# Optimization experiments

Measured on AMD Instinct MI355X. Metric: run time of the kernel, lower is better.

The kernel has to match this reference:

```python
import jax, jax.numpy as jnp
import numpy as np

DIM = 256
NUM_HEADS = 8
HEAD_DIM = DIM // NUM_HEADS
CPB_HIDDEN = 512
B, N = 2, 2304
TABLE = 9025  # (2*48-1)**2


def _l2norm(t, eps=1e-12):
    # matches torch F.normalize(dim=-1): x / max(||x||, eps)
    n = jnp.sqrt(jnp.sum(t * t, axis=-1, keepdims=True))
    return t / jnp.maximum(n, eps)


def setup_inputs() -> dict:
    key = jax.random.key(0)
    ks = jax.random.split(key, 12)
    x = jax.random.normal(ks[0], (B, N, DIM), dtype=jnp.float32)
    relative_pos_index = jax.random.randint(ks[1], (N, N), 0, TABLE, dtype=jnp.int64)
    relative_coords_table = jax.random.uniform(ks[2], (TABLE, 2), dtype=jnp.float32) * 2.0 - 1.0
    seq_length_scale = jnp.ones((1,), dtype=jnp.float32) * jnp.log2(jnp.float32(N))
    padding_mask = jnp.zeros((B, N), dtype=jnp.int32)
    s = 0.02
    W_qkv = jax.random.normal(ks[3], (3 * DIM, DIM), dtype=jnp.float32) * s
    b_qkv = jnp.zeros((3 * DIM,), dtype=jnp.float32)
    # temperature init: log(exp(1/0.24) - 1) so softplus(temperature) = 1/0.24
    temperature = jnp.full((NUM_HEADS, 1, 1), float(np.log(np.expm1(1.0 / 0.24))), dtype=jnp.float32)
    query_embedding = jax.random.normal(ks[4], (NUM_HEADS, 1, HEAD_DIM), dtype=jnp.float32) * s
    W_proj = jax.random.normal(ks[5], (DIM, DIM), dtype=jnp.float32) * s
    b_proj = jnp.zeros((DIM,), dtype=jnp.float32)
    W_cpb1 = jax.random.normal(ks[6], (CPB_HIDDEN, 2), dtype=jnp.float32) * s
    b_cpb1 = jnp.zeros((CPB_HIDDEN,), dtype=jnp.float32)
    W_cpb2 = jax.random.normal(ks[7], (NUM_HEADS, CPB_HIDDEN), dtype=jnp.float32) * s
    b_cpb2 = jnp.zeros((NUM_HEADS,), dtype=jnp.float32)
    return {
        'x': x, 'relative_pos_index': relative_pos_index,
        'relative_coords_table': relative_coords_table,
        'seq_length_scale': seq_length_scale, 'padding_mask': padding_mask,
        'W_qkv': W_qkv, 'b_qkv': b_qkv, 'temperature': temperature,
        'query_embedding': query_embedding, 'W_proj': W_proj, 'b_proj': b_proj,
        'W_cpb1': W_cpb1, 'b_cpb1': b_cpb1, 'W_cpb2': W_cpb2, 'b_cpb2': b_cpb2,
    }


def reference(x, relative_pos_index, relative_coords_table, seq_length_scale,
              padding_mask, W_qkv, b_qkv, temperature, query_embedding,
              W_proj, b_proj, W_cpb1, b_cpb1, W_cpb2, b_cpb2):
    Bx, Nx, C = x.shape
    h, d = NUM_HEADS, HEAD_DIM
    # qkv projection -> (B, 3h, N, d); first h heads = q, then k, then v
    qkv = (jnp.einsum('bnc,oc->bno', x, W_qkv) + b_qkv)
    qkv = qkv.reshape(Bx, Nx, 3 * h, d).transpose(0, 2, 1, 3)
    q, k, v = qkv[:, :h], qkv[:, h:2 * h], qkv[:, 2 * h:]
    # CPB relative bias: (T,2) -> (T,h) -> (h,N,N) via gather
    hid = jax.nn.relu(relative_coords_table @ W_cpb1.T + b_cpb1)
    tab = hid @ W_cpb2.T + b_cpb2                    # (T, h)
    rel_bias = tab.T[:, relative_pos_index.reshape(-1)].reshape(h, Nx, Nx)
    # cosine-sim attention with learned query embedding + softplus temperature
    scale = jax.nn.softplus(temperature) * seq_length_scale[0]   # (h,1,1)
    qn = (_l2norm(q) + query_embedding) * scale                  # (B,h,N,d)
    kn = _l2norm(k)
    attn = jnp.einsum('bhnd,bhmd->bhnm', qn, kn) + rel_bias
    attn = jax.nn.softmax(attn, axis=-1)
    out = jnp.einsum('bhnm,bhmd->bhnd', attn, v)
    out = out.transpose(0, 2, 1, 3).reshape(Bx, Nx, C)
    out = out @ W_proj.T + b_proj
    return out
```

## Files before the change

### kernel.cpp

```cpp
#include <hip/hip_runtime.h>
#include <math.h>

#define DIMC 256
#define NHEADS 8
#define HDIM 32
#define CPBH 512
#define BB 2
#define NSEQ 2304
#define TAB 9025
#define TABP 9040
#define RTOT (BB*NHEADS*NSEQ)
#define SPLITS 8
#define MSP (NSEQ/SPLITS)
#define PBS 36
#define NCHUNK (NSEQ/32)
#define LOG2E 1.44269504088896340736f

#define NX  (BB*NSEQ*DIMC)
#define NWQ (3*DIMC*DIMC)
#define NWP (DIMC*DIMC)

#define WSPLIT_BLOCKS ((NWQ + NWP) / 1024)
#define IDXP_ELEMS    (NSEQ * NCHUNK * 16)
#define IDXP4_BLOCKS  (IDXP_ELEMS / 1024)
#define CPB_BLOCKS    ((TAB + 63) / 64)

typedef unsigned short ushort;
typedef __attribute__((ext_vector_type(8))) short short8;
typedef __attribute__((ext_vector_type(4))) short short4v;
typedef __attribute__((ext_vector_type(4))) float f32x4;

#define MFMA16(a,b,c) __builtin_amdgcn_mfma_f32_16x16x32_bf16((a),(b),(c),0,0,0)

__device__ __forceinline__ ushort f2bf(float x) {
  unsigned u = __float_as_uint(x);
  u += 0x7FFFu + ((u >> 16) & 1u);
  return (ushort)(u >> 16);
}
__device__ __forceinline__ float bf2f(ushort b) {
  return __uint_as_float(((unsigned)b) << 16);
}
__device__ __forceinline__ float fexp2(float x) {
#if defined(__has_builtin)
#if __has_builtin(__builtin_amdgcn_exp2f)
  return __builtin_amdgcn_exp2f(x);
#else
  return exp2f(x);
#endif
#else
  return exp2f(x);
#endif
}
__device__ __forceinline__ unsigned pack_trunc(float p0, float p1) {
  return __builtin_amdgcn_perm(__float_as_uint(p1), __float_as_uint(p0), 0x07060302u);
}
__device__ __forceinline__ void cvt8(const float* __restrict__ p, short8* hi, short8* lo) {
  float4 v0 = *(const float4*)p;
  float4 v1 = *(const float4*)(p + 4);
  float vv[8] = {v0.x, v0.y, v0.z, v0.w, v1.x, v1.y, v1.z, v1.w};
  short8 h, l;
#pragma unroll
  for (int i = 0; i < 8; ++i) {
    ushort hh = f2bf(vv[i]);
    h[i] = (short)hh;
    l[i] = (short)f2bf(vv[i] - bf2f(hh));
  }
  *hi = h; *lo = l;
}

__global__ void setup_kernel(const float* __restrict__ wq, const float* __restrict__ wp,
                             const int* __restrict__ idx,
                             const float* __restrict__ tbl, const float* __restrict__ W1,
                             const float* __restrict__ b1, const float* __restrict__ W2,
                             const float* __restrict__ b2,
                             ushort* __restrict__ wqh, ushort* __restrict__ wql,
                             ushort* __restrict__ wph, ushort* __restrict__ wpl,
                             unsigned* __restrict__ idxP, ushort* __restrict__ tabBf) {
  __shared__ float w1b[CPBH * 4];
  __shared__ float w2t[CPBH * NHEADS];
  __shared__ float part[4][64][NHEADS];
  int blk = blockIdx.x;
  int tid = threadIdx.x;
  if (blk < CPB_BLOCKS) {
    for (int i = tid; i < CPBH; i += 256) {
      w1b[i * 4 + 0] = W1[2 * i];
      w1b[i * 4 + 1] = W1[2 * i + 1];
      w1b[i * 4 + 2] = b1[i];
      w1b[i * 4 + 3] = 0.f;
    }
    for (int i = tid; i < CPBH * NHEADS; i += 256)
      w2t[(i & (CPBH - 1)) * NHEADS + (i >> 9)] = W2[i];
    int tl = tid & 63, jc = tid >> 6;
    int t = blk * 64 + tl;
    bool valid = t < TAB;
    float c0 = 0.f, c1 = 0.f;
    if (valid) { c0 = tbl[2 * t]; c1 = tbl[2 * t + 1]; }
    __syncthreads();
    float acc[NHEADS];
#pragma unroll
    for (int h = 0; h < NHEADS; ++h) acc[h] = 0.f;
    for (int j = jc * 128; j < jc * 128 + 128; ++j) {
      float4 wv = *(const float4*)&w1b[j * 4];
      float hid = fmaxf(fmaf(c0, wv.x, fmaf(c1, wv.y, wv.z)), 0.f);
      float4 wa = *(const float4*)&w2t[j * NHEADS];
      float4 wb = *(const float4*)&w2t[j * NHEADS + 4];
      acc[0] = fmaf(hid, wa.x, acc[0]);
      acc[1] = fmaf(hid, wa.y, acc[1]);
      acc[2] = fmaf(hid, wa.z, acc[2]);
      acc[3] = fmaf(hid, wa.w, acc[3]);
      acc[4] = fmaf(hid, wb.x, acc[4]);
      acc[5] = fmaf(hid, wb.y, acc[5]);
      acc[6] = fmaf(hid, wb.z, acc[6]);
      acc[7] = fmaf(hid, wb.w, acc[7]);
    }
#pragma unroll
    for (int h = 0; h < NHEADS; ++h) part[jc][tl][h] = acc[h];
    __syncthreads();
    if (jc == 0 && valid) {
#pragma unroll
      for (int h = 0; h < NHEADS; ++h) {
        float s = part[0][tl][h] + part[1][tl][h] + part[2][tl][h] + part[3][tl][h] + b2[h];
        tabBf[h * TABP + t] = f2bf(s * LOG2E);
      }
    }
  } else if (blk < CPB_BLOCKS + WSPLIT_BLOCKS) {
    int i = ((blk - CPB_BLOCKS) * 256 + tid) * 4;
    const float* src; ushort *hi, *lo; int j;
    if (i < NWQ) { src = wq; hi = wqh; lo = wql; j = i; }
    else         { src = wp; hi = wph; lo = wpl; j = i - NWQ; }
    float4 v = *(const float4*)&src[j];
    ushort h0 = f2bf(v.x), h1 = f2bf(v.y), h2 = f2bf(v.z), h3 = f2bf(v.w);
    uint2 hp, lp;
    hp.x = (unsigned)h0 | ((unsigned)h1 << 16);
    hp.y = (unsigned)h2 | ((unsigned)h3 << 16);
    lp.x = (unsigned)f2bf(v.x - bf2f(h0)) | ((unsigned)f2bf(v.y - bf2f(h1)) << 16);
    lp.y = (unsigned)f2bf(v.z - bf2f(h2)) | ((unsigned)f2bf(v.w - bf2f(h3)) << 16);
    *(uint2*)&hi[j] = hp;
    *(uint2*)&lo[j] = lp;
  } else {
    int t4 = (blk - CPB_BLOCKS - WSPLIT_BLOCKS) * 256 + tid;
    int cc4 = (t4 & 3) * 4;
    int ch = (t4 >> 2) % NCHUNK;
    int n = t4 / (4 * NCHUNK);
    int mbase = ch * 32 + cc4;
    int4 a = *(const int4*)&idx[(size_t)n * NSEQ + mbase];
    int4 b = *(const int4*)&idx[(size_t)n * NSEQ + mbase + 16];
    uint4 o;
    o.x = (unsigned)a.x | ((unsigned)b.x << 16);
    o.y = (unsigned)a.y | ((unsigned)b.y << 16);
    o.z = (unsigned)a.z | ((unsigned)b.z << 16);
    o.w = (unsigned)a.w | ((unsigned)b.w << 16);
    *(uint4*)&idxP[((size_t)n * NCHUNK + ch) * 16 + cc4] = o;
  }
}

__launch_bounds__(256)
__global__ void gemm_qkv(const float* __restrict__ x,
                         const ushort* __restrict__ Bh, const ushort* __restrict__ Bl,
                         const float* __restrict__ bias, const float* __restrict__ temp,
                         const float* __restrict__ sls, const float* __restrict__ qe,
                         ushort* __restrict__ qhi, ushort* __restrict__ qlo,
                         ushort* __restrict__ khi, ushort* __restrict__ klo,
                         ushort* __restrict__ vT) {
  __shared__ float vbuf[64][65];
  int tid = threadIdx.x;
  int lane = tid & 63, w = tid >> 6;
  int g = lane >> 4, c = lane & 15;
  int n0 = blockIdx.x * 64, m0 = blockIdx.y * 64;
  int mw = m0 + w * 16;
  const int K = DIMC;
  f32x4 acc[4] = {{0,0,0,0},{0,0,0,0},{0,0,0,0},{0,0,0,0}};
#pragma unroll 2
  for (int k0 = 0; k0 < K; k0 += 32) {
    short8 ah, al;
    cvt8(&x[(size_t)(mw + c) * K + k0 + g * 8], &ah, &al);
#pragma unroll
    for (int nt = 0; nt < 4; ++nt) {
      short8 bh = *(const short8*)&Bh[(size_t)(n0 + nt * 16 + c) * K + k0 + g * 8];
      short8 bl = *(const short8*)&Bl[(size_t)(n0 + nt * 16 + c) * K + k0 + g * 8];
      acc[nt] = MFMA16(ah, bh, acc[nt]);
      acc[nt] = MFMA16(al, bh, acc[nt]);
      acc[nt] = MFMA16(ah, bl, acc[nt]);
    }
  }
#pragma unroll
  for (int nt = 0; nt < 4; ++nt) {
    float bv = bias[n0 + nt * 16 + c];
#pragma unroll
    for (int r = 0; r < 4; ++r) acc[nt][r] += bv;
  }

  int b = (m0 >= NSEQ) ? 1 : 0;
  int nb = m0 - b * NSEQ;
  int sect = n0 >> 8;
  int hloc = (n0 & 255) >> 5;

  if (sect < 2) {
#pragma unroll
    for (int H = 0; H < 2; ++H) {
      int head = hloc + H;
      float scale = (sect == 0) ? log1pf(expf(temp[head])) * sls[0] * LOG2E : 0.f;
#pragma unroll
      for (int r = 0; r < 4; ++r) {
        float ss = acc[2*H][r]*acc[2*H][r] + acc[2*H+1][r]*acc[2*H+1][r];
        ss += __shfl_xor(ss, 1);
        ss += __shfl_xor(ss, 2);
        ss += __shfl_xor(ss, 4);
        ss += __shfl_xor(ss, 8);
        float inv = 1.f / fmaxf(sqrtf(ss), 1e-12f);
#pragma unroll
        for (int half = 0; half < 2; ++half) {
          int d = half * 16 + c;
          float val = acc[2*H + half][r] * inv;
          if (sect == 0) val = (val + qe[head * HDIM + d]) * scale;
          vbuf[w * 16 + g * 4 + r][H * 32 + d] = val;
        }
      }
    }
    __syncthreads();
    int plane = tid >> 7;
    int seg = tid & 127;
    int head = seg >> 6, row = seg & 63;
    const float* srcrow = &vbuf[row][head * 32];
    ushort out16[32];
#pragma unroll
    for (int i = 0; i < 32; ++i) {
      float v = srcrow[i];
      ushort hh = f2bf(v);
      out16[i] = plane ? f2bf(v - bf2f(hh)) : hh;
    }
    ushort* dstp = plane ? (sect == 0 ? qlo : klo) : (sect == 0 ? qhi : khi);
    size_t off = ((size_t)(b * NHEADS + hloc + head) * NSEQ + nb + row) * HDIM;
#pragma unroll
    for (int q4 = 0; q4 < 4; ++q4)
      *(int4*)&dstp[off + q4 * 8] = ((int4*)out16)[q4];
  } else {
#pragma unroll
    for (int nt = 0; nt < 4; ++nt)
#pragma unroll
      for (int r = 0; r < 4; ++r)
        vbuf[w * 16 + g * 4 + r][nt * 16 + c] = acc[nt][r];
    __syncthreads();
    int hbase = (n0 - 512) >> 5;
#pragma unroll
    for (int it = 0; it < 16; ++it) {
      int dloc = (tid >> 6) * 16 + it;
      int p = tid & 63;
      int pp = p & 31;
      int nsrc = (p & 32) + (pp & 1) * 16 + (pp >> 1);
      float v = vbuf[nsrc][dloc];
      int head = hbase + (dloc >> 5), d = dloc & 31;
      vT[((size_t)((b * NHEADS + head) * HDIM + d)) * NSEQ + nb + p] = f2bf(v);
    }
  }
}

__launch_bounds__(256)
__global__ void attn_kernel(const ushort* __restrict__ qhi, const ushort* __restrict__ qlo,
                            const ushort* __restrict__ khi, const ushort* __restrict__ klo,
                            const ushort* __restrict__ vT, const ushort* __restrict__ tabBf,
                            const unsigned* __restrict__ idxP,
                            float* __restrict__ pO, float* __restrict__ pL) {
  __shared__ ushort tbf[10240];
  __shared__ __align__(16) ushort pbuf[8][16 * PBS];
  int tid = threadIdx.x;
  int lane = tid & 63;
  int w = tid >> 6;
  int qb = blockIdx.x;
  int by = blockIdx.y;
  int s = by & 7, bh = by >> 3;
  int h = bh & (NHEADS - 1);

  const ushort* tsrc = tabBf + h * TABP;
#pragma unroll
  for (int i = 0; i < 5; ++i) {
    int off = i * 2048 + tid * 8;
    *(int4*)&tbf[off] = *(const int4*)&tsrc[off];
  }

  int g = lane >> 4, c = lane & 15;
  int q0 = qb * 128 + w * 16;
  int q1 = q0 + 64;
  size_t rowbase = (size_t)bh * NSEQ;

  short8 qAh = *(const short8*)&qhi[(rowbase + q0 + c) * HDIM + g * 8];
  short8 qAl = *(const short8*)&qlo[(rowbase + q0 + c) * HDIM + g * 8];
  short8 qBh = *(const short8*)&qhi[(rowbase + q1 + c) * HDIM + g * 8];
  short8 qBl = *(const short8*)&qlo[(rowbase + q1 + c) * HDIM + g * 8];
  __syncthreads();

  short one = (c == 0) ? (short)0x3F80 : (short)0;
  short8 onesB = {one, one, one, one, one, one, one, one};

  f32x4 oa0 = {0,0,0,0}, oa1 = {0,0,0,0}, ob0 = {0,0,0,0}, ob1 = {0,0,0,0};
  f32x4 la = {0,0,0,0}, lb = {0,0,0,0};
  ushort* pba = pbuf[w * 2];
  ushort* pbb = pbuf[w * 2 + 1];
  int m0 = s * MSP;

#define LOADK(MT, D0H, D0L, D1H, D1L, IA0, IA1, IA2, IA3, IB0, IB1, IB2, IB3) do { \
    size_t ra_ = (rowbase + (MT) + c) * HDIM + g * 8;                 \
    D0H = *(const short8*)&khi[ra_];                                  \
    D0L = *(const short8*)&klo[ra_];                                  \
    D1H = *(const short8*)&khi[ra_ + 16 * HDIM];                      \
    D1L = *(const short8*)&klo[ra_ + 16 * HDIM];                      \
    size_t ia_ = ((size_t)(q0 + g * 4) * NCHUNK + ((MT) >> 5)) * 16 + c; \
    IA0 = idxP[ia_];                                                  \
    IA1 = idxP[ia_ + (size_t)NCHUNK * 16];                            \
    IA2 = idxP[ia_ + (size_t)2 * NCHUNK * 16];                        \
    IA3 = idxP[ia_ + (size_t)3 * NCHUNK * 16];                        \
    size_t ibx_ = ((size_t)(q1 + g * 4) * NCHUNK + ((MT) >> 5)) * 16 + c; \
    IB0 = idxP[ibx_];                                                 \
    IB1 = idxP[ibx_ + (size_t)NCHUNK * 16];                           \
    IB2 = idxP[ibx_ + (size_t)2 * NCHUNK * 16];                       \
    IB3 = idxP[ibx_ + (size_t)3 * NCHUNK * 16];                       \
  } while (0)

  short8 c0h, c0l, c1h, c1l;
  unsigned ia0, ia1, ia2, ia3, ib0, ib1, ib2, ib3;
  LOADK(m0, c0h, c0l, c1h, c1l, ia0, ia1, ia2, ia3, ib0, ib1, ib2, ib3);

  for (int mt = m0; mt < m0 + MSP; mt += 32) {
    int mtn = (mt + 32 < m0 + MSP) ? (mt + 32) : m0;
    short8 n0h, n0l, n1h, n1l;
    unsigned ja0, ja1, ja2, ja3, jb0, jb1, jb2, jb3;
    LOADK(mtn, n0h, n0l, n1h, n1l, ja0, ja1, ja2, ja3, jb0, jb1, jb2, jb3);

    f32x4 sa0 = {0,0,0,0}, sa1 = {0,0,0,0}, sb0 = {0,0,0,0}, sb1 = {0,0,0,0};
    sa0 = MFMA16(qAh, c0h, sa0);
    sb0 = MFMA16(qBh, c0h, sb0);
    sa1 = MFMA16(qAh, c1h, sa1);
    sb1 = MFMA16(qBh, c1h, sb1);
    sa0 = MFMA16(qAl, c0h, sa0);
    sb0 = MFMA16(qBl, c0h, sb0);
    sa1 = MFMA16(qAl, c1h, sa1);
    sb1 = MFMA16(qBl, c1h, sb1);
    sa0 = MFMA16(qAh, c0l, sa0);
    sb0 = MFMA16(qBh, c0l, sb0);
    sa1 = MFMA16(qAh, c1l, sa1);
    sb1 = MFMA16(qBh, c1l, sb1);

    size_t va = ((size_t)(bh * HDIM + c)) * NSEQ + mt + g * 8;
    short8 vf0 = *(const short8*)&vT[va];
    short8 vf1 = *(const short8*)&vT[va + 16 * NSEQ];

    unsigned ipa[4] = {ia0, ia1, ia2, ia3};
    unsigned ipb[4] = {ib0, ib1, ib2, ib3};
#pragma unroll
    for (int r = 0; r < 4; ++r) {
      int k0 = ipa[r] & 0xFFFF, k1 = ipa[r] >> 16;
      float pA0 = fexp2(sa0[r] + bf2f(tbf[k0]));
      float pA1 = fexp2(sa1[r] + bf2f(tbf[k1]));
      *(unsigned*)&pba[(g * 4 + r) * PBS + 2 * c] = pack_trunc(pA0, pA1);
    }
#pragma unroll
    for (int r = 0; r < 4; ++r) {
      int k0 = ipb[r] & 0xFFFF, k1 = ipb[r] >> 16;
      float pB0 = fexp2(sb0[r] + bf2f(tbf[k0]));
      float pB1 = fexp2(sb1[r] + bf2f(tbf[k1]));
      *(unsigned*)&pbb[(g * 4 + r) * PBS + 2 * c] = pack_trunc(pB0, pB1);
    }

    short4v paA = *(const short4v*)&pba[c * PBS + g * 8];
    short4v paB = *(const short4v*)&pba[c * PBS + g * 8 + 4];
    short8 pfa = __builtin_shufflevector(paA, paB, 0, 1, 2, 3, 4, 5, 6, 7);
    short4v pbA = *(const short4v*)&pbb[c * PBS + g * 8];
    short4v pbB = *(const short4v*)&pbb[c * PBS + g * 8 + 4];
    short8 pfb = __builtin_shufflevector(pbA, pbB, 0, 1, 2, 3, 4, 5, 6, 7);

    oa0 = MFMA16(pfa, vf0, oa0);
    oa1 = MFMA16(pfa, vf1, oa1);
    ob0 = MFMA16(pfb, vf0, ob0);
    ob1 = MFMA16(pfb, vf1, ob1);
    la  = MFMA16(pfa, onesB, la);
    lb  = MFMA16(pfb, onesB, lb);

    c0h = n0h; c0l = n0l; c1h = n1h; c1l = n1l;
    ia0 = ja0; ia1 = ja1; ia2 = ja2; ia3 = ja3;
    ib0 = jb0; ib1 = jb1; ib2 = jb2; ib3 = jb3;
  }
#undef LOADK

  size_t prow0 = (size_t)s * RTOT + rowbase;
#pragma unroll
  for (int r = 0; r < 4; ++r) {
    size_t pra = prow0 + q0 + g * 4 + r;
    pO[pra * HDIM + c]      = oa0[r];
    pO[pra * HDIM + 16 + c] = oa1[r];
    size_t prb = prow0 + q1 + g * 4 + r;
    pO[prb * HDIM + c]      = ob0[r];
    pO[prb * HDIM + 16 + c] = ob1[r];
    if (c == 0) { pL[pra] = la[r]; pL[prb] = lb[r]; }
  }
}

#define ALD 264
__launch_bounds__(256)
__global__ void gemm_proj_fused(const float* __restrict__ pO, const float* __restrict__ pL,
                                const ushort* __restrict__ Bh_, const ushort* __restrict__ Bl_,
                                const float* __restrict__ bias, float* __restrict__ C) {
  __shared__ __align__(16) ushort Ahs[64 * ALD];
  __shared__ __align__(16) ushort Als[64 * ALD];
  int tid = threadIdx.x;
  int m0 = blockIdx.x * 64;
  int b = (m0 >= NSEQ) ? 1 : 0;
  int nb = m0 - b * NSEQ;

  {
    int r = tid >> 2;
    int q = tid & 3;
    int n = nb + r;
#pragma unroll
    for (int h = 0; h < NHEADS; ++h) {
      size_t bhn = (size_t)(b * NHEADS + h) * NSEQ + n;
      float L = 0.f;
#pragma unroll
      for (int sp = 0; sp < SPLITS; ++sp) L += pL[(size_t)sp * RTOT + bhn];
      float inv = 1.f / L;
      float a[8] = {0.f, 0.f, 0.f, 0.f, 0.f, 0.f, 0.f, 0.f};
#pragma unroll
      for (int sp = 0; sp < SPLITS; ++sp) {
        const float* src = &pO[((size_t)sp * RTOT + bhn) * HDIM + q * 8];
        float4 v0 = *(const float4*)&src[0];
        float4 v1 = *(const float4*)&src[4];
        a[0] += v0.x; a[1] += v0.y; a[2] += v0.z; a[3] += v0.w;
        a[4] += v1.x; a[5] += v1.y; a[6] += v1.z; a[7] += v1.w;
      }
      ushort hi8[8], lo8[8];
#pragma unroll
      for (int i = 0; i < 8; ++i) {
        float v = a[i] * inv;
        ushort hh = f2bf(v);
        hi8[i] = hh;
        lo8[i] = f2bf(v - bf2f(hh));
      }
      int k = h * 32 + q * 8;
      *(int4*)&Ahs[r * ALD + k] = *(int4*)hi8;
      *(int4*)&Als[r * ALD + k] = *(int4*)lo8;
    }
  }
  __syncthreads();

  int lane = tid & 63, w = tid >> 6;
  int g = lane >> 4, c = lane & 15;
  int n0 = w * 64;
  f32x4 acc[4][4] = {};
  for (int k0 = 0; k0 < DIMC; k0 += 32) {
    short8 bfh[4], bfl[4];
#pragma unroll
    for (int nt = 0; nt < 4; ++nt) {
      bfh[nt] = *(const short8*)&Bh_[(size_t)(n0 + nt * 16 + c) * DIMC + k0 + g * 8];
      bfl[nt] = *(const short8*)&Bl_[(size_t)(n0 + nt * 16 + c) * DIMC + k0 + g * 8];
    }
#pragma unroll
    for (int mt = 0; mt < 4; ++mt) {
      short8 ah = *(const short8*)&Ahs[(mt * 16 + c) * ALD + k0 + g * 8];
      short8 al = *(const short8*)&Als[(mt * 16 + c) * ALD + k0 + g * 8];
#pragma unroll
      for (int nt = 0; nt < 4; ++nt) {
        acc[mt][nt] = MFMA16(ah, bfh[nt], acc[mt][nt]);
        acc[mt][nt] = MFMA16(al, bfh[nt], acc[mt][nt]);
        acc[mt][nt] = MFMA16(ah, bfl[nt], acc[mt][nt]);
      }
    }
  }
#pragma unroll
  for (int nt = 0; nt < 4; ++nt) {
    float bv = bias[n0 + nt * 16 + c];
#pragma unroll
    for (int mt = 0; mt < 4; ++mt)
#pragma unroll
      for (int r = 0; r < 4; ++r)
        C[(size_t)(m0 + mt * 16 + g * 4 + r) * DIMC + n0 + nt * 16 + c] = acc[mt][nt][r] + bv;
  }
}

extern "C" void kernel_launch(void* const* d_in, const int* in_sizes, int n_in,
                              void* d_out, int out_size, void* d_ws, size_t ws_size,
                              hipStream_t stream) {
  const float* x    = (const float*)d_in[0];
  const int*   idx  = (const int*)d_in[1];
  const float* tbl  = (const float*)d_in[2];
  const float* sls  = (const float*)d_in[3];
  const float* Wqkv = (const float*)d_in[5];
  const float* bqkv = (const float*)d_in[6];
  const float* temp = (const float*)d_in[7];
  const float* qe   = (const float*)d_in[8];
  const float* Wp   = (const float*)d_in[9];
  const float* bp   = (const float*)d_in[10];
  const float* W1   = (const float*)d_in[11];
  const float* b1   = (const float*)d_in[12];
  const float* W2   = (const float*)d_in[13];
  const float* b2   = (const float*)d_in[14];

  float* ws   = (float*)d_ws;
  float* pO   = ws;
  float* pL   = pO + (size_t)SPLITS * RTOT * HDIM;
  unsigned* idxP = (unsigned*)(pL + (size_t)SPLITS * RTOT);
  ushort* u   = (ushort*)(idxP + IDXP_ELEMS);
  ushort* qhi = u;                u += (size_t)RTOT * HDIM;
  ushort* qlo = u;                u += (size_t)RTOT * HDIM;
  ushort* khi = u;                u += (size_t)RTOT * HDIM;
  ushort* klo = u;                u += (size_t)RTOT * HDIM;
  ushort* vT  = u;                u += (size_t)RTOT * HDIM;
  ushort* wqh = u;                u += NWQ;
  ushort* wql = u;                u += NWQ;
  ushort* wph = u;                u += NWP;
  ushort* wpl = u;                u += NWP;
  ushort* tabBf = u;              u += 73728;
  float* out  = (float*)d_out;

  setup_kernel<<<dim3(CPB_BLOCKS + WSPLIT_BLOCKS + IDXP4_BLOCKS), dim3(256), 0, stream>>>(
      Wqkv, Wp, idx, tbl, W1, b1, W2, b2,
      wqh, wql, wph, wpl, idxP, tabBf);
  gemm_qkv<<<dim3(12, 72), dim3(256), 0, stream>>>(
      x, wqh, wql, bqkv, temp, sls, qe, qhi, qlo, khi, klo, vT);
  attn_kernel<<<dim3(NSEQ / 128, BB * NHEADS * SPLITS), dim3(256), 0, stream>>>(
      qhi, qlo, khi, klo, vT, tabBf, idxP, pO, pL);
  gemm_proj_fused<<<dim3((BB * NSEQ) / 64), dim3(256), 0, stream>>>(
      pO, pL, wph, wpl, bp, out);
}
```

Before: 220.2 us.

## Fuse QKV GEMM into setup kernel, convert weights inline, halve KV splits

Merges the CPB table, QKV GEMM and index-packing work into one pre_kernel launch, and drops the separate weight hi/lo split pass by converting fp32 weights to bf16 pairs inside both GEMM inner loops. This removes one kernel launch and the round trip of split weights through memory. It also cuts the attention split-K factor from 8 to 4, which halves partial-output traffic and reduction work but halves the attention grid's parallelism. The weight conversion is now repeated by every block that reads the weights, and the QKV GEMM can no longer start only after the CPB blocks finish, so it overlaps with them instead.

After: 215.5 us (median of 2 runs). 2.1% less time.

```diff
diff --git a/kernel.cpp b/kernel.cpp
--- a/kernel.cpp
+++ b/kernel.cpp
@@ -10,20 +10,17 @@
 #define TAB 9025
 #define TABP 9040
 #define RTOT (BB*NHEADS*NSEQ)
-#define SPLITS 8
+#define SPLITS 4
 #define MSP (NSEQ/SPLITS)
 #define PBS 36
 #define NCHUNK (NSEQ/32)
 #define LOG2E 1.44269504088896340736f
 
-#define NX  (BB*NSEQ*DIMC)
 #define NWQ (3*DIMC*DIMC)
-#define NWP (DIMC*DIMC)
-
-#define WSPLIT_BLOCKS ((NWQ + NWP) / 1024)
 #define IDXP_ELEMS    (NSEQ * NCHUNK * 16)
 #define IDXP4_BLOCKS  (IDXP_ELEMS / 1024)
 #define CPB_BLOCKS    ((TAB + 63) / 64)
+#define QKV_BLOCKS    (12 * 72)
 
 typedef unsigned short ushort;
 typedef __attribute__((ext_vector_type(8))) short short8;
@@ -68,20 +65,26 @@
   *hi = h; *lo = l;
 }
 
-__global__ void setup_kernel(const float* __restrict__ wq, const float* __restrict__ wp,
-                             const int* __restrict__ idx,
-                             const float* __restrict__ tbl, const float* __restrict__ W1,
-                             const float* __restrict__ b1, const float* __restrict__ W2,
-                             const float* __restrict__ b2,
-                             ushort* __restrict__ wqh, ushort* __restrict__ wql,
-                             ushort* __restrict__ wph, ushort* __restrict__ wpl,
-                             unsigned* __restrict__ idxP, ushort* __restrict__ tabBf) {
-  __shared__ float w1b[CPBH * 4];
-  __shared__ float w2t[CPBH * NHEADS];
-  __shared__ float part[4][64][NHEADS];
+__launch_bounds__(256)
+__global__ void pre_kernel(const float* __restrict__ x, const float* __restrict__ wq,
+                           const int* __restrict__ idx,
+                           const float* __restrict__ tbl, const float* __restrict__ W1,
+                           const float* __restrict__ b1, const float* __restrict__ W2,
+                           const float* __restrict__ b2,
+                           const float* __restrict__ bias, const float* __restrict__ temp,
+                           const float* __restrict__ sls, const float* __restrict__ qe,
+                           ushort* __restrict__ qhi, ushort* __restrict__ qlo,
+                           ushort* __restrict__ khi, ushort* __restrict__ klo,
+                           ushort* __restrict__ vT,
+                           unsigned* __restrict__ idxP, ushort* __restrict__ tabBf) {
+  __shared__ __align__(16) float smem[8192];
   int blk = blockIdx.x;
   int tid = threadIdx.x;
+
   if (blk < CPB_BLOCKS) {
+    float* w1b = smem;
+    float* w2t = smem + 2048;
+    float* part = smem + 6144;
     for (int i = tid; i < CPBH; i += 256) {
       w1b[i * 4 + 0] = W1[2 * i];
       w1b[i * 4 + 1] = W1[2 * i + 1];
@@ -114,31 +117,111 @@
       acc[7] = fmaf(hid, wb.w, acc[7]);
     }
 #pragma unroll
-    for (int h = 0; h < NHEADS; ++h) part[jc][tl][h] = acc[h];
+    for (int h = 0; h < NHEADS; ++h) part[((size_t)jc * 64 + tl) * NHEADS + h] = acc[h];
     __syncthreads();
     if (jc == 0 && valid) {
 #pragma unroll
       for (int h = 0; h < NHEADS; ++h) {
-        float s = part[0][tl][h] + part[1][tl][h] + part[2][tl][h] + part[3][tl][h] + b2[h];
+        float s = b2[h];
+#pragma unroll
+        for (int p = 0; p < 4; ++p) s += part[((size_t)p * 64 + tl) * NHEADS + h];
         tabBf[h * TABP + t] = f2bf(s * LOG2E);
       }
     }
-  } else if (blk < CPB_BLOCKS + WSPLIT_BLOCKS) {
-    int i = ((blk - CPB_BLOCKS) * 256 + tid) * 4;
-    const float* src; ushort *hi, *lo; int j;
-    if (i < NWQ) { src = wq; hi = wqh; lo = wql; j = i; }
-    else         { src = wp; hi = wph; lo = wpl; j = i - NWQ; }
-    float4 v = *(const float4*)&src[j];
-    ushort h0 = f2bf(v.x), h1 = f2bf(v.y), h2 = f2bf(v.z), h3 = f2bf(v.w);
-    uint2 hp, lp;
-    hp.x = (unsigned)h0 | ((unsigned)h1 << 16);
-    hp.y = (unsigned)h2 | ((unsigned)h3 << 16);
-    lp.x = (unsigned)f2bf(v.x - bf2f(h0)) | ((unsigned)f2bf(v.y - bf2f(h1)) << 16);
-    lp.y = (unsigned)f2bf(v.z - bf2f(h2)) | ((unsigned)f2bf(v.w - bf2f(h3)) << 16);
-    *(uint2*)&hi[j] = hp;
-    *(uint2*)&lo[j] = lp;
+  } else if (blk < CPB_BLOCKS + QKV_BLOCKS) {
+    float (*vbuf)[65] = (float(*)[65])smem;
+    int t = blk - CPB_BLOCKS;
+    int n0 = (t % 12) * 64, m0 = (t / 12) * 64;
+    int lane = tid & 63, w = tid >> 6;
+    int g = lane >> 4, c = lane & 15;
+    int mw = m0 + w * 16;
+    const int K = DIMC;
+    f32x4 acc[4] = {{0,0,0,0},{0,0,0,0},{0,0,0,0},{0,0,0,0}};
+#pragma unroll 2
+    for (int k0 = 0; k0 < K; k0 += 32) {
+      short8 ah, al;
+      cvt8(&x[(size_t)(mw + c) * K + k0 + g * 8], &ah, &al);
+#pragma unroll
+      for (int nt = 0; nt < 4; ++nt) {
+        short8 bh, bl;
+        cvt8(&wq[(size_t)(n0 + nt * 16 + c) * K + k0 + g * 8], &bh, &bl);
+        acc[nt] = MFMA16(ah, bh, acc[nt]);
+        acc[nt] = MFMA16(al, bh, acc[nt]);
+        acc[nt] = MFMA16(ah, bl, acc[nt]);
+      }
+    }
+#pragma unroll
+    for (int nt = 0; nt < 4; ++nt) {
+      float bv = bias[n0 + nt * 16 + c];
+#pragma unroll
+      for (int r = 0; r < 4; ++r) acc[nt][r] += bv;
+    }
+
+    int b = (m0 >= NSEQ) ? 1 : 0;
+    int nb = m0 - b * NSEQ;
+    int sect = n0 >> 8;
+    int hloc = (n0 & 255) >> 5;
+
+    if (sect < 2) {
+#pragma unroll
+      for (int H = 0; H < 2; ++H) {
+        int head = hloc + H;
+        float scale = (sect == 0) ? log1pf(expf(temp[head])) * sls[0] * LOG2E : 0.f;
+#pragma unroll
+        for (int r = 0; r < 4; ++r) {
+          float ss = acc[2*H][r]*acc[2*H][r] + acc[2*H+1][r]*acc[2*H+1][r];
+          ss += __shfl_xor(ss, 1);
+          ss += __shfl_xor(ss, 2);
+          ss += __shfl_xor(ss, 4);
+          ss += __shfl_xor(ss, 8);
+          float inv = 1.f / fmaxf(sqrtf(ss), 1e-12f);
+#pragma unroll
+          for (int half = 0; half < 2; ++half) {
+            int d = half * 16 + c;
+            float val = acc[2*H + half][r] * inv;
+            if (sect == 0) val = (val + qe[head * HDIM + d]) * scale;
+            vbuf[w * 16 + g * 4 + r][H * 32 + d] = val;
+          }
+        }
+      }
+      __syncthreads();
+      int plane = tid >> 7;
+      int seg = tid & 127;
+      int head = seg >> 6, row = seg & 63;
+      const float* srcrow = &vbuf[row][head * 32];
+      ushort out16[32];
+#pragma unroll
+      for (int i = 0; i < 32; ++i) {
+        float v = srcrow[i];
+        ushort hh = f2bf(v);
+        out16[i] = plane ? f2bf(v - bf2f(hh)) : hh;
+      }
+      ushort* dstp = plane ? (sect == 0 ? qlo : klo) : (sect == 0 ? qhi : khi);
+      size_t off = ((size_t)(b * NHEADS + hloc + head) * NSEQ + nb + row) * HDIM;
+#pragma unroll
+      for (int q4 = 0; q4 < 4; ++q4)
+        *(int4*)&dstp[off + q4 * 8] = ((int4*)out16)[q4];
+    } else {
+#pragma unroll
+      for (int nt = 0; nt < 4; ++nt)
+#pragma unroll
+        for (int r = 0; r < 4; ++r)
+          vbuf[w * 16 + g * 4 + r][nt * 16 + c] = acc[nt][r];
+      __syncthreads();
+      int hbase = (n0 - 512) >> 5;
+#pragma unroll
+      for (int it = 0; it < 16; ++it) {
+        int dloc = (tid >> 6) * 16 + it;
+        int p = tid & 63;
+        int pp = p & 31;
+        int nsrc = (p & 32) + (pp & 1) * 16 + (pp >> 1);
+        float v = vbuf[nsrc][dloc];
+        int head = hbase + (dloc >> 5), d = dloc & 31;
+        vT[((size_t)((b * NHEADS + head) * HDIM + d)) * NSEQ + nb + p] = f2bf(v);
+      }
+    }
   } else {
-    int t4 = (blk - CPB_BLOCKS - WSPLIT_BLOCKS) * 256 + tid;
+    int t4 = (blk - CPB_BLOCKS - QKV_BLOCKS) * 256 + tid;
     int cc4 = (t4 & 3) * 4;
     int ch = (t4 >> 2) % NCHUNK;
     int n = t4 / (4 * NCHUNK);
@@ -151,107 +234,6 @@
     o.z = (unsigned)a.z | ((unsigned)b.z << 16);
     o.w = (unsigned)a.w | ((unsigned)b.w << 16);
     *(uint4*)&idxP[((size_t)n * NCHUNK + ch) * 16 + cc4] = o;
-  }
-}
-
-__launch_bounds__(256)
-__global__ void gemm_qkv(const float* __restrict__ x,
-                         const ushort* __restrict__ Bh, const ushort* __restrict__ Bl,
-                         const float* __restrict__ bias, const float* __restrict__ temp,
-                         const float* __restrict__ sls, const float* __restrict__ qe,
-                         ushort* __restrict__ qhi, ushort* __restrict__ qlo,
-                         ushort* __restrict__ khi, ushort* __restrict__ klo,
-                         ushort* __restrict__ vT) {
-  __shared__ float vbuf[64][65];
-  int tid = threadIdx.x;
-  int lane = tid & 63, w = tid >> 6;
-  int g = lane >> 4, c = lane & 15;
-  int n0 = blockIdx.x * 64, m0 = blockIdx.y * 64;
-  int mw = m0 + w * 16;
-  const int K = DIMC;
-  f32x4 acc[4] = {{0,0,0,0},{0,0,0,0},{0,0,0,0},{0,0,0,0}};
-#pragma unroll 2
-  for (int k0 = 0; k0 < K; k0 += 32) {
-    short8 ah, al;
-    cvt8(&x[(size_t)(mw + c) * K + k0 + g * 8], &ah, &al);
-#pragma unroll
-    for (int nt = 0; nt < 4; ++nt) {
-      short8 bh = *(const short8*)&Bh[(size_t)(n0 + nt * 16 + c) * K + k0 + g * 8];
-      short8 bl = *(const short8*)&Bl[(size_t)(n0 + nt * 16 + c) * K + k0 + g * 8];
-      acc[nt] = MFMA16(ah, bh, acc[nt]);
-      acc[nt] = MFMA16(al, bh, acc[nt]);
-      acc[nt] = MFMA16(ah, bl, acc[nt]);
-    }
-  }
-#pragma unroll
-  for (int nt = 0; nt < 4; ++nt) {
-    float bv = bias[n0 + nt * 16 + c];
-#pragma unroll
-    for (int r = 0; r < 4; ++r) acc[nt][r] += bv;
-  }
-
-  int b = (m0 >= NSEQ) ? 1 : 0;
-  int nb = m0 - b * NSEQ;
-  int sect = n0 >> 8;
-  int hloc = (n0 & 255) >> 5;
-
-  if (sect < 2) {
-#pragma unroll
-    for (int H = 0; H < 2; ++H) {
-      int head = hloc + H;
-      float scale = (sect == 0) ? log1pf(expf(temp[head])) * sls[0] * LOG2E : 0.f;
-#pragma unroll
-      for (int r = 0; r < 4; ++r) {
-        float ss = acc[2*H][r]*acc[2*H][r] + acc[2*H+1][r]*acc[2*H+1][r];
-        ss += __shfl_xor(ss, 1);
-        ss += __shfl_xor(ss, 2);
-        ss += __shfl_xor(ss, 4);
-        ss += __shfl_xor(ss, 8);
-        float inv = 1.f / fmaxf(sqrtf(ss), 1e-12f);
-#pragma unroll
-        for (int half = 0; half < 2; ++half) {
-          int d = half * 16 + c;
-          float val = acc[2*H + half][r] * inv;
-          if (sect == 0) val = (val + qe[head * HDIM + d]) * scale;
-          vbuf[w * 16 + g * 4 + r][H * 32 + d] = val;
-        }
-      }
-    }
-    __syncthreads();
-    int plane = tid >> 7;
-    int seg = tid & 127;
-    int head = seg >> 6, row = seg & 63;
-    const float* srcrow = &vbuf[row][head * 32];
-    ushort out16[32];
-#pragma unroll
-    for (int i = 0; i < 32; ++i) {
-      float v = srcrow[i];
-      ushort hh = f2bf(v);
-      out16[i] = plane ? f2bf(v - bf2f(hh)) : hh;
-    }
-    ushort* dstp = plane ? (sect == 0 ? qlo : klo) : (sect == 0 ? qhi : khi);
-    size_t off = ((size_t)(b * NHEADS + hloc + head) * NSEQ + nb + row) * HDIM;
-#pragma unroll
-    for (int q4 = 0; q4 < 4; ++q4)
-      *(int4*)&dstp[off + q4 * 8] = ((int4*)out16)[q4];
-  } else {
-#pragma unroll
-    for (int nt = 0; nt < 4; ++nt)
-#pragma unroll
-      for (int r = 0; r < 4; ++r)
-        vbuf[w * 16 + g * 4 + r][nt * 16 + c] = acc[nt][r];
-    __syncthreads();
-    int hbase = (n0 - 512) >> 5;
-#pragma unroll
-    for (int it = 0; it < 16; ++it) {
-      int dloc = (tid >> 6) * 16 + it;
-      int p = tid & 63;
-      int pp = p & 31;
-      int nsrc = (p & 32) + (pp & 1) * 16 + (pp >> 1);
-      float v = vbuf[nsrc][dloc];
-      int head = hbase + (dloc >> 5), d = dloc & 31;
-      vT[((size_t)((b * NHEADS + head) * HDIM + d)) * NSEQ + nb + p] = f2bf(v);
-    }
   }
 }
 
@@ -268,7 +250,7 @@
   int w = tid >> 6;
   int qb = blockIdx.x;
   int by = blockIdx.y;
-  int s = by & 7, bh = by >> 3;
+  int s = by & 3, bh = by >> 2;
   int h = bh & (NHEADS - 1);
 
   const ushort* tsrc = tabBf + h * TABP;
@@ -397,7 +379,7 @@
 #define ALD 264
 __launch_bounds__(256)
 __global__ void gemm_proj_fused(const float* __restrict__ pO, const float* __restrict__ pL,
-                                const ushort* __restrict__ Bh_, const ushort* __restrict__ Bl_,
+                                const float* __restrict__ Wp,
                                 const float* __restrict__ bias, float* __restrict__ C) {
   __shared__ __align__(16) ushort Ahs[64 * ALD];
   __shared__ __align__(16) ushort Als[64 * ALD];
@@ -448,10 +430,8 @@
   for (int k0 = 0; k0 < DIMC; k0 += 32) {
     short8 bfh[4], bfl[4];
 #pragma unroll
-    for (int nt = 0; nt < 4; ++nt) {
-      bfh[nt] = *(const short8*)&Bh_[(size_t)(n0 + nt * 16 + c) * DIMC + k0 + g * 8];
-      bfl[nt] = *(const short8*)&Bl_[(size_t)(n0 + nt * 16 + c) * DIMC + k0 + g * 8];
-    }
+    for (int nt = 0; nt < 4; ++nt)
+      cvt8(&Wp[(size_t)(n0 + nt * 16 + c) * DIMC + k0 + g * 8], &bfh[nt], &bfl[nt]);
 #pragma unroll
     for (int mt = 0; mt < 4; ++mt) {
       short8 ah = *(const short8*)&Ahs[(mt * 16 + c) * ALD + k0 + g * 8];
@@ -503,20 +483,14 @@
   ushort* khi = u;                u += (size_t)RTOT * HDIM;
   ushort* klo = u;                u += (size_t)RTOT * HDIM;
   ushort* vT  = u;                u += (size_t)RTOT * HDIM;
-  ushort* wqh = u;                u += NWQ;
-  ushort* wql = u;                u += NWQ;
-  ushort* wph = u;                u += NWP;
-  ushort* wpl = u;                u += NWP;
   ushort* tabBf = u;              u += 73728;
   float* out  = (float*)d_out;
 
-  setup_kernel<<<dim3(CPB_BLOCKS + WSPLIT_BLOCKS + IDXP4_BLOCKS), dim3(256), 0, stream>>>(
-      Wqkv, Wp, idx, tbl, W1, b1, W2, b2,
-      wqh, wql, wph, wpl, idxP, tabBf);
-  gemm_qkv<<<dim3(12, 72), dim3(256), 0, stream>>>(
-      x, wqh, wql, bqkv, temp, sls, qe, qhi, qlo, khi, klo, vT);
+  pre_kernel<<<dim3(CPB_BLOCKS + QKV_BLOCKS + IDXP4_BLOCKS), dim3(256), 0, stream>>>(
+      x, Wqkv, idx, tbl, W1, b1, W2, b2, bqkv, temp, sls, qe,
+      qhi, qlo, khi, klo, vT, idxP, tabBf);
   attn_kernel<<<dim3(NSEQ / 128, BB * NHEADS * SPLITS), dim3(256), 0, stream>>>(
       qhi, qlo, khi, klo, vT, tabBf, idxP, pO, pL);
   gemm_proj_fused<<<dim3((BB * NSEQ) / 64), dim3(256), 0, stream>>>(
-      pO, pL, wph, wpl, bp, out);
-}
+      pO, pL, Wp, bp, out);
+}
```
